# Optimization experiments

Hardware: AMD Instinct MI355X
Metric: run time of the kernel (lower is better)

Reference implementation:

```python
import jax, jax.numpy as jnp
import numpy as np

B, L, D, H, K = 64, 512, 768, 768, 128


def setup_inputs() -> dict:
    key = jax.random.key(0)
    ks = jax.random.split(key, 8)
    enc = jax.random.normal(ks[0], (B, L, D), dtype=jnp.float32)
    valid_mask = jax.random.randint(ks[1], (B, L), 0, 2)
    pos_span = jnp.sort(jax.random.randint(ks[2], (B, 2), 0, 40), axis=-1)
    mask_span = jax.random.randint(ks[3], (B,), 0, L)
    s1 = 1.0 / np.sqrt(D)
    s2 = 1.0 / np.sqrt(H)
    W1 = jax.random.normal(ks[4], (D, H), dtype=jnp.float32) * s1
    b1 = jax.random.normal(ks[5], (H,), dtype=jnp.float32) * s1
    W2 = jax.random.normal(ks[6], (H, K), dtype=jnp.float32) * s2
    b2 = jax.random.normal(ks[7], (K,), dtype=jnp.float32) * s2
    return {"encoder_layers": enc, "W1": W1, "b1": b1, "W2": W2, "b2": b2,
            "valid_mask": valid_mask, "pos_span": pos_span, "mask_span": mask_span}


def _pretrained_feature(enc, valid_mask, pos_span, mask_span):
    # mask_feat: gather token at mask_span[i] per row -> [B, D]
    mask_feat = enc[jnp.arange(B), mask_span]
    # Compact valid tokens to the front of each row (stable order).
    v = valid_mask == 1                               # [B, L]
    pos = jnp.cumsum(v.astype(jnp.int32), axis=1) - 1  # compacted dest index
    dest = jnp.where(v, pos, L)                        # invalid tokens -> slot L (dropped)
    valid_output = jnp.zeros((B, L + 1, D), dtype=enc.dtype)
    valid_output = valid_output.at[jnp.arange(B)[:, None], dest].set(enc)
    valid_output = valid_output[:, :L]                 # rest stays zero, as in torch
    # Span-wise max pool over compacted positions [start, end] inclusive.
    p = jnp.arange(L)[None, :]
    span = (p >= pos_span[:, 0:1]) & (p <= pos_span[:, 1:2])  # [B, L]
    neg_inf = jnp.array(-jnp.inf, dtype=enc.dtype)
    feat = jnp.max(jnp.where(span[:, :, None], valid_output, neg_inf), axis=1)
    return feat, mask_feat


def reference(encoder_layers, W1, b1, W2, b2, valid_mask, pos_span, mask_span):
    feat, _mask_feat = _pretrained_feature(encoder_layers, valid_mask, pos_span, mask_span)
    # head: Linear -> ReLU -> Dropout(eval: identity) -> Linear
    h = jax.nn.relu(feat @ W1 + b1)
    logits = h @ W2 + b2
    return logits
```

## Files before the change

kernel.cpp:

```cpp
#include <hip/hip_runtime.h>
#include <math.h>

#define BB 64
#define LL 512
#define DD 768
#define HH 768
#define KK 128

static __device__ __forceinline__ float4 fmax4(float4 a, float4 b) {
    float4 r;
    r.x = fmaxf(a.x, b.x); r.y = fmaxf(a.y, b.y);
    r.z = fmaxf(a.z, b.z); r.w = fmaxf(a.w, b.w);
    return r;
}

#define FEAT_OFF 0
#define H_OFF    (BB * DD)

__global__ __launch_bounds__(512) void halton_feat_kernel(
    const float* __restrict__ enc,
    const int*   __restrict__ valid_mask,
    const int*   __restrict__ pos_span,
    float*       __restrict__ feat)
{
    __shared__ int    s_idx[40];
    __shared__ int    s_count;
    __shared__ float4 s_red[8][64];

    const int b    = blockIdx.x;
    const int part = blockIdx.y;
    const int tid  = threadIdx.x;

    const int lo = pos_span[b * 2 + 0];
    const int hi = pos_span[b * 2 + 1];

    if (tid < 64) {
        int v[8];
        #pragma unroll
        for (int c = 0; c < 8; ++c)
            v[c] = valid_mask[b * LL + c * 64 + tid];
        int count = 0;
        #pragma unroll
        for (int c = 0; c < 8; ++c) {
            unsigned long long mk = __ballot(v[c] == 1);
            if (v[c] == 1) {
                int rank = count + __popcll(mk & ((1ull << tid) - 1ull));
                if (rank < 40) s_idx[rank] = c * 64 + tid;
            }
            count += __popcll(mk);
        }
        if (tid == 0) s_count = count;
    }
    __syncthreads();

    const int count = s_count;
    const int pend  = min(hi, count - 1);

    const int c4   = tid & 63;
    const int g    = tid >> 6;
    const int fcol = part * 64 + c4;

    float4 m = make_float4(-INFINITY, -INFINITY, -INFINITY, -INFINITY);
    for (int p = lo + g; p <= pend; p += 8) {
        m = fmax4(m, ((const float4*)&enc[((long)b * LL + s_idx[p]) * DD])[fcol]);
    }
    if (hi >= count) m = fmax4(m, make_float4(0.f, 0.f, 0.f, 0.f));
    s_red[g][c4] = m;
    __syncthreads();

    if (g == 0) {
        float4 r = s_red[0][c4];
        #pragma unroll
        for (int q = 1; q < 8; ++q) r = fmax4(r, s_red[q][c4]);
        ((float4*)&feat[(long)b * DD])[fcol] = r;
    }
}

__global__ __launch_bounds__(512) void halton_gemm1_kernel(
    const float* __restrict__ feat,
    const float* __restrict__ W1,
    const float* __restrict__ b1,
    float*       __restrict__ h)
{
    __shared__ float s_feat[2 * DD];
    __shared__ float s_part[8][2][128];

    const int tid   = threadIdx.x;
    const int jbase = blockIdx.x * 128;
    const int bbase = blockIdx.y * 2;
    const int lane  = tid & 63;
    const int w     = tid >> 6;

    {
        const float4* src = (const float4*)&feat[bbase * DD];
        float4*       dst = (float4*)s_feat;
        for (int i = tid; i < 2 * DD / 4; i += 512) dst[i] = src[i];
    }
    __syncthreads();

    const int j0 = jbase + lane;
    const int j1 = j0 + 64;
    const float4* f40 = (const float4*)&s_feat[0];
    const float4* f41 = (const float4*)&s_feat[DD];

    float a00 = 0.f, a01 = 0.f, a10 = 0.f, a11 = 0.f;
    #pragma unroll 4
    for (int k4 = 0; k4 < 24; ++k4) {
        const int kf = w * 24 + k4;
        const int k  = kf * 4;
        const float4 fv0 = f40[kf];
        const float4 fv1 = f41[kf];
        const float w00 = W1[(k + 0) * HH + j0];
        const float w01 = W1[(k + 0) * HH + j1];
        const float w10 = W1[(k + 1) * HH + j0];
        const float w11 = W1[(k + 1) * HH + j1];
        const float w20 = W1[(k + 2) * HH + j0];
        const float w21 = W1[(k + 2) * HH + j1];
        const float w30 = W1[(k + 3) * HH + j0];
        const float w31 = W1[(k + 3) * HH + j1];
        a00 += fv0.x * w00 + fv0.y * w10 + fv0.z * w20 + fv0.w * w30;
        a01 += fv0.x * w01 + fv0.y * w11 + fv0.z * w21 + fv0.w * w31;
        a10 += fv1.x * w00 + fv1.y * w10 + fv1.z * w20 + fv1.w * w30;
        a11 += fv1.x * w01 + fv1.y * w11 + fv1.z * w21 + fv1.w * w31;
    }
    s_part[w][0][lane]      = a00;
    s_part[w][0][lane + 64] = a01;
    s_part[w][1][lane]      = a10;
    s_part[w][1][lane + 64] = a11;
    __syncthreads();

    if (tid < 256) {
        const int bl  = tid >> 7;
        const int col = tid & 127;
        float r = b1[jbase + col];
        #pragma unroll
        for (int q = 0; q < 8; ++q) r += s_part[q][bl][col];
        h[(long)(bbase + bl) * HH + jbase + col] = fmaxf(r, 0.f);
    }
}

__global__ __launch_bounds__(384) void halton_gemm2_kernel(
    const float* __restrict__ h,
    const float* __restrict__ W2,
    const float* __restrict__ b2,
    float*       __restrict__ out)
{
    __shared__ float s_h[HH];
    __shared__ float s_part[6][64];

    const int tid = threadIdx.x;
    const int b   = blockIdx.y;
    const int col = blockIdx.x * 64 + (tid & 63);
    const int seg = tid >> 6;

    if (tid < HH / 4)
        ((float4*)s_h)[tid] = ((const float4*)&h[(long)b * HH])[tid];
    __syncthreads();

    float a0 = 0.f, a1 = 0.f, a2 = 0.f, a3 = 0.f;
    #pragma unroll 4
    for (int i4 = 0; i4 < 32; ++i4) {
        const int k = seg * 128 + i4 * 4;
        const float4 hv = *(const float4*)&s_h[k];
        a0 += hv.x * W2[(k + 0) * KK + col];
        a1 += hv.y * W2[(k + 1) * KK + col];
        a2 += hv.z * W2[(k + 2) * KK + col];
        a3 += hv.w * W2[(k + 3) * KK + col];
    }
    s_part[seg][tid & 63] = (a0 + a1) + (a2 + a3);
    __syncthreads();

    if (tid < 64) {
        float r = b2[col];
        #pragma unroll
        for (int q = 0; q < 6; ++q) r += s_part[q][tid];
        out[b * KK + col] = r;
    }
}

extern "C" void kernel_launch(void* const* d_in, const int* in_sizes, int n_in,
                              void* d_out, int out_size, void* d_ws, size_t ws_size,
                              hipStream_t stream) {
    const float* enc        = (const float*)d_in[0];
    const float* W1         = (const float*)d_in[1];
    const float* b1         = (const float*)d_in[2];
    const float* W2         = (const float*)d_in[3];
    const float* b2         = (const float*)d_in[4];
    const int*   valid_mask = (const int*)d_in[5];
    const int*   pos_span   = (const int*)d_in[6];
    float* out  = (float*)d_out;
    float* feat = (float*)d_ws + FEAT_OFF;
    float* h    = (float*)d_ws + H_OFF;

    halton_feat_kernel<<<dim3(BB, 3), 512, 0, stream>>>(enc, valid_mask, pos_span, feat);
    halton_gemm1_kernel<<<dim3(6, 32), 512, 0, stream>>>(feat, W1, b1, h);
    halton_gemm2_kernel<<<dim3(2, BB), 384, 0, stream>>>(h, W2, b2, out);
}
```

Before: 20.08 us.

## Fuse span max-pool feature extraction into the first GEMM kernel

Merges the feature-gather/max-pool kernel into the first MLP GEMM kernel. Each block recomputes the compacted indices and span max for its two batch rows in shared memory, then runs the GEMM directly from shared memory. This drops one kernel launch and the global round trip for feat. The cost is redundant work: each batch row's pooling is repeated across the 6 column blocks, so enc rows are read 6 times, though likely from L2. The pooling loop is also unrolled two-way across rows.

```diff
diff --git a/kernel.cpp b/kernel.cpp
--- a/kernel.cpp
+++ b/kernel.cpp
@@ -14,76 +14,19 @@
     return r;
 }
 
-#define FEAT_OFF 0
-#define H_OFF    (BB * DD)
-
-__global__ __launch_bounds__(512) void halton_feat_kernel(
+__global__ __launch_bounds__(512) void halton_featmlp_kernel(
     const float* __restrict__ enc,
+    const float* __restrict__ W1,
+    const float* __restrict__ b1,
     const int*   __restrict__ valid_mask,
     const int*   __restrict__ pos_span,
-    float*       __restrict__ feat)
-{
-    __shared__ int    s_idx[40];
-    __shared__ int    s_count;
-    __shared__ float4 s_red[8][64];
-
-    const int b    = blockIdx.x;
-    const int part = blockIdx.y;
-    const int tid  = threadIdx.x;
-
-    const int lo = pos_span[b * 2 + 0];
-    const int hi = pos_span[b * 2 + 1];
-
-    if (tid < 64) {
-        int v[8];
-        #pragma unroll
-        for (int c = 0; c < 8; ++c)
-            v[c] = valid_mask[b * LL + c * 64 + tid];
-        int count = 0;
-        #pragma unroll
-        for (int c = 0; c < 8; ++c) {
-            unsigned long long mk = __ballot(v[c] == 1);
-            if (v[c] == 1) {
-                int rank = count + __popcll(mk & ((1ull << tid) - 1ull));
-                if (rank < 40) s_idx[rank] = c * 64 + tid;
-            }
-            count += __popcll(mk);
-        }
-        if (tid == 0) s_count = count;
-    }
-    __syncthreads();
-
-    const int count = s_count;
-    const int pend  = min(hi, count - 1);
-
-    const int c4   = tid & 63;
-    const int g    = tid >> 6;
-    const int fcol = part * 64 + c4;
-
-    float4 m = make_float4(-INFINITY, -INFINITY, -INFINITY, -INFINITY);
-    for (int p = lo + g; p <= pend; p += 8) {
-        m = fmax4(m, ((const float4*)&enc[((long)b * LL + s_idx[p]) * DD])[fcol]);
-    }
-    if (hi >= count) m = fmax4(m, make_float4(0.f, 0.f, 0.f, 0.f));
-    s_red[g][c4] = m;
-    __syncthreads();
-
-    if (g == 0) {
-        float4 r = s_red[0][c4];
-        #pragma unroll
-        for (int q = 1; q < 8; ++q) r = fmax4(r, s_red[q][c4]);
-        ((float4*)&feat[(long)b * DD])[fcol] = r;
-    }
-}
-
-__global__ __launch_bounds__(512) void halton_gemm1_kernel(
-    const float* __restrict__ feat,
-    const float* __restrict__ W1,
-    const float* __restrict__ b1,
     float*       __restrict__ h)
 {
-    __shared__ float s_feat[2 * DD];
-    __shared__ float s_part[8][2][128];
+    __shared__ int    s_idx[2][40];
+    __shared__ int    s_count[2];
+    __shared__ float4 s_red[4][2][192];
+    __shared__ float  s_feat[2][DD];
+    __shared__ float  s_part[8][2][128];
 
     const int tid   = threadIdx.x;
     const int jbase = blockIdx.x * 128;
@@ -91,42 +34,101 @@
     const int lane  = tid & 63;
     const int w     = tid >> 6;
 
-    {
-        const float4* src = (const float4*)&feat[bbase * DD];
-        float4*       dst = (float4*)s_feat;
-        for (int i = tid; i < 2 * DD / 4; i += 512) dst[i] = src[i];
+    if (w < 2) {
+        const int b = bbase + w;
+        int v[8];
+        #pragma unroll
+        for (int c = 0; c < 8; ++c)
+            v[c] = valid_mask[b * LL + c * 64 + lane];
+        int count = 0;
+        #pragma unroll
+        for (int c = 0; c < 8; ++c) {
+            unsigned long long mk = __ballot(v[c] == 1);
+            if (v[c] == 1) {
+                int rank = count + __popcll(mk & ((1ull << lane) - 1ull));
+                if (rank < 40) s_idx[w][rank] = c * 64 + lane;
+            }
+            count += __popcll(mk);
+        }
+        if (lane == 0) s_count[w] = count;
     }
     __syncthreads();
 
-    const int j0 = jbase + lane;
-    const int j1 = j0 + 64;
-    const float4* f40 = (const float4*)&s_feat[0];
-    const float4* f41 = (const float4*)&s_feat[DD];
+    {
+        const int bl = w & 1;
+        const int g  = w >> 1;
+        const int b  = bbase + bl;
+        const int lo = pos_span[b * 2 + 0];
+        const int hi = pos_span[b * 2 + 1];
+        const int count = s_count[bl];
+        const int pend  = min(hi, count - 1);
 
-    float a00 = 0.f, a01 = 0.f, a10 = 0.f, a11 = 0.f;
-    #pragma unroll 4
-    for (int k4 = 0; k4 < 24; ++k4) {
-        const int kf = w * 24 + k4;
-        const int k  = kf * 4;
-        const float4 fv0 = f40[kf];
-        const float4 fv1 = f41[kf];
-        const float w00 = W1[(k + 0) * HH + j0];
-        const float w01 = W1[(k + 0) * HH + j1];
-        const float w10 = W1[(k + 1) * HH + j0];
-        const float w11 = W1[(k + 1) * HH + j1];
-        const float w20 = W1[(k + 2) * HH + j0];
-        const float w21 = W1[(k + 2) * HH + j1];
-        const float w30 = W1[(k + 3) * HH + j0];
-        const float w31 = W1[(k + 3) * HH + j1];
-        a00 += fv0.x * w00 + fv0.y * w10 + fv0.z * w20 + fv0.w * w30;
-        a01 += fv0.x * w01 + fv0.y * w11 + fv0.z * w21 + fv0.w * w31;
-        a10 += fv1.x * w00 + fv1.y * w10 + fv1.z * w20 + fv1.w * w30;
-        a11 += fv1.x * w01 + fv1.y * w11 + fv1.z * w21 + fv1.w * w31;
+        const float4 ninf = make_float4(-INFINITY, -INFINITY, -INFINITY, -INFINITY);
+        float4 m0 = ninf, m1 = ninf, m2 = ninf;
+        float4 n0 = ninf, n1 = ninf, n2 = ninf;
+        for (int p = lo + g; p <= pend; p += 8) {
+            const float4* r4 = (const float4*)&enc[((long)b * LL + s_idx[bl][p]) * DD];
+            m0 = fmax4(m0, r4[lane]);
+            m1 = fmax4(m1, r4[lane + 64]);
+            m2 = fmax4(m2, r4[lane + 128]);
+            if (p + 4 <= pend) {
+                const float4* q4 = (const float4*)&enc[((long)b * LL + s_idx[bl][p + 4]) * DD];
+                n0 = fmax4(n0, q4[lane]);
+                n1 = fmax4(n1, q4[lane + 64]);
+                n2 = fmax4(n2, q4[lane + 128]);
+            }
+        }
+        m0 = fmax4(m0, n0); m1 = fmax4(m1, n1); m2 = fmax4(m2, n2);
+        if (hi >= count) {
+            const float4 z = make_float4(0.f, 0.f, 0.f, 0.f);
+            m0 = fmax4(m0, z); m1 = fmax4(m1, z); m2 = fmax4(m2, z);
+        }
+        s_red[g][bl][lane]       = m0;
+        s_red[g][bl][lane + 64]  = m1;
+        s_red[g][bl][lane + 128] = m2;
     }
-    s_part[w][0][lane]      = a00;
-    s_part[w][0][lane + 64] = a01;
-    s_part[w][1][lane]      = a10;
-    s_part[w][1][lane + 64] = a11;
+    __syncthreads();
+
+    if ((w & 3) != 3) {
+        const int bl = w >> 2;
+        const int fc = (w & 3) * 64 + lane;
+        float4 r = fmax4(fmax4(s_red[0][bl][fc], s_red[1][bl][fc]),
+                         fmax4(s_red[2][bl][fc], s_red[3][bl][fc]));
+        ((float4*)&s_feat[bl][0])[fc] = r;
+    }
+    __syncthreads();
+
+    {
+        const int j0 = jbase + lane;
+        const int j1 = j0 + 64;
+        const float4* f40 = (const float4*)&s_feat[0][0];
+        const float4* f41 = (const float4*)&s_feat[1][0];
+
+        float a00 = 0.f, a01 = 0.f, a10 = 0.f, a11 = 0.f;
+        #pragma unroll 4
+        for (int k4 = 0; k4 < 24; ++k4) {
+            const int kf = w * 24 + k4;
+            const int k  = kf * 4;
+            const float4 fv0 = f40[kf];
+            const float4 fv1 = f41[kf];
+            const float w00 = W1[(k + 0) * HH + j0];
+            const float w01 = W1[(k + 0) * HH + j1];
+            const float w10 = W1[(k + 1) * HH + j0];
+            const float w11 = W1[(k + 1) * HH + j1];
+            const float w20 = W1[(k + 2) * HH + j0];
+            const float w21 = W1[(k + 2) * HH + j1];
+            const float w30 = W1[(k + 3) * HH + j0];
+            const float w31 = W1[(k + 3) * HH + j1];
+            a00 += fv0.x * w00 + fv0.y * w10 + fv0.z * w20 + fv0.w * w30;
+            a01 += fv0.x * w01 + fv0.y * w11 + fv0.z * w21 + fv0.w * w31;
+            a10 += fv1.x * w00 + fv1.y * w10 + fv1.z * w20 + fv1.w * w30;
+            a11 += fv1.x * w01 + fv1.y * w11 + fv1.z * w21 + fv1.w * w31;
+        }
+        s_part[w][0][lane]      = a00;
+        s_part[w][0][lane + 64] = a01;
+        s_part[w][1][lane]      = a10;
+        s_part[w][1][lane + 64] = a11;
+    }
     __syncthreads();
 
     if (tid < 256) {
@@ -188,11 +190,10 @@
     const float* b2         = (const float*)d_in[4];
     const int*   valid_mask = (const int*)d_in[5];
     const int*   pos_span   = (const int*)d_in[6];
-    float* out  = (float*)d_out;
-    float* feat = (float*)d_ws + FEAT_OFF;
-    float* h    = (float*)d_ws + H_OFF;
+    float* out = (float*)d_out;
+    float* h   = (float*)d_ws;
 
-    halton_feat_kernel<<<dim3(BB, 3), 512, 0, stream>>>(enc, valid_mask, pos_span, feat);
-    halton_gemm1_kernel<<<dim3(6, 32), 512, 0, stream>>>(feat, W1, b1, h);
+    halton_featmlp_kernel<<<dim3(6, 32), 512, 0, stream>>>(enc, W1, b1,
+                                                           valid_mask, pos_span, h);
     halton_gemm2_kernel<<<dim3(2, BB), 384, 0, stream>>>(h, W2, b2, out);
 }
```

Measured after the change: 20.29 us. About the same (+1.0%).
